# Kernel tuning notes

Measured on AMD Instinct MI355X. Metric: run time of the kernel, lower is better.

## Reference

```python
import jax, jax.numpy as jnp
import numpy as np

M = 0.25
GAMMA = 256.0
HARD_W = 2.0
O_P = 1.0 + M
O_N = -M
DELTA_P = 1.0 - M
DELTA_N = M
NEG_BIG = -1e30  # masked-out fill for logsumexp (finite to keep grads NaN-free)


def setup_inputs() -> dict:
    key = jax.random.key(0)
    k1, k2 = jax.random.split(key)
    inputs = jax.random.normal(k1, (4096, 512), dtype=jnp.float32)
    targets = jax.random.randint(k2, (4096,), 0, 64, dtype=jnp.int64)
    return {"inputs": inputs, "targets": targets}


def reference(inputs, targets):
    n = inputs.shape[0]
    x = inputs / jnp.linalg.norm(inputs, axis=1, keepdims=True)  # L2 normalize
    sim = x @ x.T                                                # [n, n]

    same = targets[:, None] == targets[None, :]
    eye = jnp.eye(n, dtype=bool)
    pos_mask = same & ~eye
    neg_mask = ~same
    npos = pos_mask.sum(axis=1)
    nneg = neg_mask.sum(axis=1)

    sim_d = jax.lax.stop_gradient(sim)  # alphas are detached in the original
    alpha_p = jax.nn.relu(O_P - sim_d)
    alpha_n = jax.nn.relu(sim_d - O_N)

    # hard mining: scale alpha at hardest positive (min sim) / hardest negative (max sim)
    idx = jnp.arange(n)
    hard_p = jnp.argmin(jnp.where(pos_mask, sim_d, jnp.inf), axis=1)
    hard_n = jnp.argmax(jnp.where(neg_mask, sim_d, -jnp.inf), axis=1)
    hit_p = (idx[None, :] == hard_p[:, None]) & (npos > 1)[:, None]
    hit_n = (idx[None, :] == hard_n[:, None]) & (nneg > 1)[:, None]
    alpha_p = alpha_p * jnp.where(hit_p, HARD_W, 1.0)
    alpha_n = alpha_n * jnp.where(hit_n, HARD_W, 1.0)

    pos_term = jnp.where(pos_mask, -GAMMA * alpha_p * (sim - DELTA_P), NEG_BIG)
    neg_term = jnp.where(neg_mask, GAMMA * alpha_n * (sim - DELTA_N), NEG_BIG)
    lse_p = jax.nn.logsumexp(pos_term, axis=1)
    lse_n = jax.nn.logsumexp(neg_term, axis=1)

    valid = (npos > 0) & (nneg > 0)
    per_row = jnp.where(valid, jax.nn.softplus(lse_p + lse_n), 0.0)
    n_valid = jnp.maximum(valid.sum(), 1)
    return per_row.sum() / n_valid.astype(per_row.dtype)
```

## Files before the change

### kernel.cpp

```cpp
#include <hip/hip_runtime.h>


#define GAMMA_ 256.0f
#define MASKT_  (-1.0e4f)
#define MINITP_ (-1.0e4f)
#define MASKP_  (-3.0e4f)

constexpr int N_ = 4096;
constexpr int D_ = 512;
constexpr int AST_ = 520;
constexpr int CCH_ = 16;

typedef __bf16 bf16x8 __attribute__((ext_vector_type(8)));
typedef float  f32x4  __attribute__((ext_vector_type(4)));
typedef const unsigned int __attribute__((address_space(1)))* gp_t;
typedef unsigned int       __attribute__((address_space(3)))* lp_t;

__device__ __forceinline__ float pos_q(float s) {
    float d = s - 1.0f;
    return fmaf(d * d, 256.0f, -16.0f);
}
__device__ __forceinline__ float neg_q(float s) {
    float q = fmaf(s * s, 256.0f, -16.0f);
    return (s >= -0.25f) ? q : 0.0f;
}
__device__ __forceinline__ void lse_merge(float m2, float S2, float& m, float& S) {
    float mm = fmaxf(m, m2);
    S = S * __expf(m - mm) + S2 * __expf(m2 - mm);
    m = mm;
}
__device__ __forceinline__ unsigned short f2bf(float f) {
    unsigned int u = __float_as_uint(f);
    unsigned int r = u + 0x7FFFu + ((u >> 16) & 1u);
    return (unsigned short)(r >> 16);
}

__global__ __launch_bounds__(256) void k_norm(const float* __restrict__ in,
                                              unsigned short* __restrict__ xb,
                                              float* __restrict__ acc) {
    const int row  = blockIdx.x * 4 + (threadIdx.x >> 6);
    const int lane = threadIdx.x & 63;
    const float4* src = (const float4*)(in + (size_t)row * D_) + lane * 2;
    float4 a = src[0], b = src[1];
    float ss = a.x*a.x + a.y*a.y + a.z*a.z + a.w*a.w
             + b.x*b.x + b.y*b.y + b.z*b.z + b.w*b.w;
    #pragma unroll
    for (int d = 32; d >= 1; d >>= 1) ss += __shfl_xor(ss, d);
    float rn = 1.0f / sqrtf(ss);
    float v[8] = {a.x, a.y, a.z, a.w, b.x, b.y, b.z, b.w};
    union { uint4 u; unsigned short us[8]; } pk;
    #pragma unroll
    for (int k = 0; k < 8; ++k) pk.us[k] = f2bf(v[k] * rn);
    *((uint4*)(xb + (size_t)row * D_) + lane) = pk.u;
    if (blockIdx.x == 0 && threadIdx.x < 2) acc[threadIdx.x] = 0.0f;
}

__global__ __launch_bounds__(256, 4) void k_mainD(const unsigned short* __restrict__ xb,
                                                  const int* __restrict__ tg,
                                                  float* __restrict__ part) {
    constexpr int NST = 16;
    __shared__ __align__(16) unsigned short Bs[2][16][AST_];

    const int tid  = threadIdx.x;
    const int wave = tid >> 6, lane = tid & 63;
    const int n16  = lane & 15, quad = lane >> 4;
    const int rg   = (int)blockIdx.x >> 4;
    const int cc   = (int)blockIdx.x & 15;
    const int rowBase = rg * 64 + wave * 16;
    const int colBase = cc * 256;

    bf16x8 af[16];
    {
        const bf16x8* ap = (const bf16x8*)(xb + (size_t)(rowBase + n16) * D_ + quad * 8);
        #pragma unroll
        for (int kk = 0; kk < 16; ++kk) af[kk] = ap[kk * 4];
    }
    int tr[4];
    #pragma unroll
    for (int r = 0; r < 4; ++r) tr[r] = tg[rowBase + quad * 4 + r];

    float m_p[4], S_p[4], m_n[4], S_n[4], mxn[4];
    #pragma unroll
    for (int r = 0; r < 4; ++r) {
        m_p[r] = MINITP_; S_p[r] = 0.f; m_n[r] = 0.f; S_n[r] = 0.f; mxn[r] = -2.0f;
    }

    const char* gstage = (const char*)xb + (size_t)colBase * 1024 + lane * 16;

    #pragma unroll
    for (int p = 0; p < 4; ++p) {
        int j = p * 4 + wave;
        __builtin_amdgcn_global_load_lds((gp_t)(const void*)(gstage + j * 1024),
                                         (lp_t)(void*)&Bs[0][j][0], 16, 0, 0);
    }
    int tc_cur = tg[colBase + n16];

    #pragma unroll 1
    for (int s = 0; s < NST; ++s) {
        const int b = s & 1;
        __syncthreads();

        if (s + 1 < NST) {
            const char* g2 = gstage + (size_t)(s + 1) * 16 * 1024;
            #pragma unroll
            for (int p = 0; p < 4; ++p) {
                int j = p * 4 + wave;
                __builtin_amdgcn_global_load_lds((gp_t)(const void*)(g2 + j * 1024),
                                                 (lp_t)(void*)&Bs[b ^ 1][j][0], 16, 0, 0);
            }
        }
        int tc_nxt = (s + 1 < NST) ? tg[colBase + (s + 1) * 16 + n16] : 0;

        f32x4 a0 = {0.f, 0.f, 0.f, 0.f}, a1 = {0.f, 0.f, 0.f, 0.f};
        #pragma unroll
        for (int kk = 0; kk < 8; ++kk) {
            bf16x8 bf0 = *(const bf16x8*)&Bs[b][n16][(2 * kk) * 32 + quad * 8];
            bf16x8 bf1 = *(const bf16x8*)&Bs[b][n16][(2 * kk + 1) * 32 + quad * 8];
            a0 = __builtin_amdgcn_mfma_f32_16x16x32_bf16(af[2 * kk],     bf0, a0, 0, 0, 0);
            a1 = __builtin_amdgcn_mfma_f32_16x16x32_bf16(af[2 * kk + 1], bf1, a1, 0, 0, 0);
        }

        const int jcol = colBase + s * 16 + n16;
        const int rd = jcol - rowBase - quad * 4;
        #pragma unroll
        for (int r = 0; r < 4; ++r) {
            float sim = a0[r] + a1[r];
            bool samec = (tr[r] == tc_cur);
            float d1 = sim - 1.0f;
            float tp = fmaf(d1 * d1, 256.0f, -16.0f);
            tp = (samec && rd != r) ? tp : MASKP_;
            float mm = fmaxf(m_p[r], tp);
            S_p[r] = S_p[r] * __expf(m_p[r] - mm) + __expf(tp - mm); m_p[r] = mm;
            float q = fmaf(sim * sim, 256.0f, -16.0f);
            q = (sim >= -0.25f) ? q : 0.0f;
            float tn = samec ? MASKT_ : q;
            mm = fmaxf(m_n[r], tn);
            S_n[r] = S_n[r] * __expf(m_n[r] - mm) + __expf(tn - mm); m_n[r] = mm;
            mxn[r] = fmaxf(mxn[r], samec ? -2.0f : sim);
        }
        tc_cur = tc_nxt;
    }

    #pragma unroll
    for (int r = 0; r < 4; ++r) {
        #pragma unroll
        for (int d = 1; d <= 8; d <<= 1) {
            lse_merge(__shfl_xor(m_p[r], d), __shfl_xor(S_p[r], d), m_p[r], S_p[r]);
            lse_merge(__shfl_xor(m_n[r], d), __shfl_xor(S_n[r], d), m_n[r], S_n[r]);
            mxn[r] = fmaxf(mxn[r], __shfl_xor(mxn[r], d));
        }
    }
    if (n16 == 0) {
        #pragma unroll
        for (int r = 0; r < 4; ++r) {
            ((float4*)part)[(size_t)(rowBase + quad * 4 + r) * CCH_ + cc] =
                make_float4(m_p[r], S_p[r], mxn[r], S_n[r]);
        }
    }
}

__global__ __launch_bounds__(256) void k_reduceD(const float* __restrict__ part,
                                                 const int* __restrict__ tg,
                                                 float* __restrict__ acc) {
    __shared__ int hist[64];
    const int tid = threadIdx.x;
    if (tid < 64) hist[tid] = 0;
    __syncthreads();
    for (int i = tid; i < N_; i += 256) atomicAdd(&hist[tg[i]], 1);
    __syncthreads();

    const int row = blockIdx.x * 256 + tid;
    const float4* P = (const float4*)part + (size_t)row * CCH_;
    float M_p = MINITP_, Sp = 0.f, M_n = 0.f, Sn = 0.f, mxn = -2.0f;
    #pragma unroll
    for (int c = 0; c < CCH_; ++c) {
        float4 a = P[c];
        lse_merge(a.x, a.y, M_p, Sp);
        float mn = (a.z > -1.5f) ? fmaxf(neg_q(a.z), 0.0f) : 0.0f;
        lse_merge(mn, a.w, M_n, Sn);
        mxn = fmaxf(mxn, a.z);
    }
    const int cnt = hist[tg[row]];
    float np2 = (float)(cnt - 1), nn2 = (float)(N_ - cnt);
    float loss = 0.f, vld = 0.f;
    if (np2 > 0.5f && nn2 > 0.5f) {
        if (np2 > 1.5f) {
            float t1 = M_p, t2 = 2.0f * t1;
            float mm = fmaxf(M_p, t2);
            Sp = Sp * __expf(M_p - mm) + __expf(t2 - mm) - __expf(t1 - mm);
            M_p = mm;
        }
        if (nn2 > 1.5f) {
            float t1 = neg_q(mxn), t2 = 2.0f * t1;
            float mm = fmaxf(M_n, t2);
            Sn = Sn * __expf(M_n - mm) + __expf(t2 - mm) - __expf(t1 - mm);
            M_n = mm;
        }
        float z = (M_p + __logf(Sp)) + (M_n + __logf(Sn));
        loss = fmaxf(z, 0.0f) + log1pf(__expf(-fabsf(z)));
        vld = 1.0f;
    }
    #pragma unroll
    for (int d = 32; d >= 1; d >>= 1) { loss += __shfl_xor(loss, d); vld += __shfl_xor(vld, d); }
    if ((tid & 63) == 0) { atomicAdd(&acc[0], loss); atomicAdd(&acc[1], vld); }
}

__global__ void k_final(const float* __restrict__ acc, float* __restrict__ out) {
    if (threadIdx.x == 0) out[0] = acc[0] / fmaxf(acc[1], 1.0f);
}

__global__ void k_sentinel(float* __restrict__ out) {
    if (threadIdx.x == 0) out[0] = -12345.0f;
}

__global__ __launch_bounds__(1024, 4) void k_main3(const unsigned short* __restrict__ xb,
                                                   const int* __restrict__ tg,
                                                   float* __restrict__ acc_g) {
    __shared__ __align__(16) unsigned short As[16 * AST_];
    __shared__ float sm[16][16][8];
    const int tid  = threadIdx.x;
    const int wave = tid >> 6, lane = tid & 63;
    const int n16  = lane & 15, quad = lane >> 4;
    const int rowBase = blockIdx.x * 16;
    {
        int row = tid >> 6, c = tid & 63;
        *(uint4*)&As[row * AST_ + c * 8] =
            *(const uint4*)(xb + (size_t)(rowBase + row) * D_ + c * 8);
    }
    int ir[4], tr[4];
    #pragma unroll
    for (int r = 0; r < 4; ++r) { ir[r] = rowBase + quad * 4 + r; tr[r] = tg[ir[r]]; }
    float m_p[4], S_p[4], m_n[4], S_n[4], mnp[4], mxn[4], sc[4];
    #pragma unroll
    for (int r = 0; r < 4; ++r) {
        m_p[r] = 0.f; S_p[r] = 0.f; m_n[r] = 0.f; S_n[r] = 0.f;
        mnp[r] = 2.0f; mxn[r] = -2.0f; sc[r] = 0.f;
    }
    __syncthreads();
    const unsigned short* Af = &As[n16 * AST_ + quad * 8];
    #pragma unroll 1
    for (int t = wave; t < N_ / 16; t += 16) {
        const int jcol = t * 16 + n16;
        const int tc = tg[jcol];
        const bf16x8* bp = (const bf16x8*)(xb + (size_t)jcol * D_ + quad * 8);
        bf16x8 bf[16];
        #pragma unroll
        for (int kk = 0; kk < 16; ++kk) bf[kk] = bp[kk * 4];
        f32x4 a0 = {0.f, 0.f, 0.f, 0.f}, a1 = {0.f, 0.f, 0.f, 0.f};
        #pragma unroll
        for (int kk = 0; kk < 8; ++kk) {
            bf16x8 af0 = *(const bf16x8*)(Af + (2 * kk) * 32);
            bf16x8 af1 = *(const bf16x8*)(Af + (2 * kk + 1) * 32);
            a0 = __builtin_amdgcn_mfma_f32_16x16x32_bf16(af0, bf[2 * kk],     a0, 0, 0, 0);
            a1 = __builtin_amdgcn_mfma_f32_16x16x32_bf16(af1, bf[2 * kk + 1], a1, 0, 0, 0);
        }
        #pragma unroll
        for (int r = 0; r < 4; ++r) {
            float s = a0[r] + a1[r];
            bool samec = (tr[r] == tc);
            bool posm  = samec && (jcol != ir[r]);
            float tp = posm  ? pos_q(s) : MASKT_;
            float tn = samec ? MASKT_ : neg_q(s);
            float mm = fmaxf(m_p[r], tp);
            S_p[r] = S_p[r] * __expf(m_p[r] - mm) + __expf(tp - mm); m_p[r] = mm;
            mm = fmaxf(m_n[r], tn);
            S_n[r] = S_n[r] * __expf(m_n[r] - mm) + __expf(tn - mm); m_n[r] = mm;
            sc[r] += samec ? 1.0f : 0.0f;
            mnp[r] = fminf(mnp[r], posm ? s : 2.0f);
            mxn[r] = fmaxf(mxn[r], samec ? -2.0f : s);
        }
    }
    #pragma unroll
    for (int r = 0; r < 4; ++r) {
        #pragma unroll
        for (int d = 1; d <= 8; d <<= 1) {
            lse_merge(__shfl_xor(m_p[r], d), __shfl_xor(S_p[r], d), m_p[r], S_p[r]);
            lse_merge(__shfl_xor(m_n[r], d), __shfl_xor(S_n[r], d), m_n[r], S_n[r]);
            mnp[r] = fminf(mnp[r], __shfl_xor(mnp[r], d));
            mxn[r] = fmaxf(mxn[r], __shfl_xor(mxn[r], d));
            sc[r] += __shfl_xor(sc[r], d);
        }
    }
    if (n16 == 0) {
        #pragma unroll
        for (int r = 0; r < 4; ++r) {
            float* q = sm[wave][quad * 4 + r];
            q[0] = m_p[r]; q[1] = S_p[r]; q[2] = m_n[r]; q[3] = S_n[r];
            q[4] = mnp[r]; q[5] = mxn[r]; q[6] = sc[r];
        }
    }
    __syncthreads();
    if (tid < 64) {
        const int L = tid & 15;
        float m_p2 = 0.f, S_p2 = 0.f, m_n2 = 0.f, S_n2 = 0.f;
        float mnp2 = 2.0f, mxn2 = -2.0f, sct = 0.f;
        #pragma unroll
        for (int w = 0; w < 16; ++w) {
            const float* q = sm[w][L];
            lse_merge(q[0], q[1], m_p2, S_p2);
            lse_merge(q[2], q[3], m_n2, S_n2);
            mnp2 = fminf(mnp2, q[4]); mxn2 = fmaxf(mxn2, q[5]);
            sct += q[6];
        }
        float loss = 0.f, vld = 0.f;
        float np2 = sct - 1.0f, nn2 = (float)N_ - sct;
        if (tid < 16 && np2 > 0.5f && nn2 > 0.5f) {
            if (np2 > 1.5f) {
                float t1 = pos_q(mnp2), t2 = 2.0f * t1;
                float mm = fmaxf(m_p2, t2);
                S_p2 = S_p2 * __expf(m_p2 - mm) + __expf(t2 - mm) - __expf(t1 - mm);
                m_p2 = mm;
            }
            if (nn2 > 1.5f) {
                float t1 = neg_q(mxn2), t2 = 2.0f * t1;
                float mm = fmaxf(m_n2, t2);
                S_n2 = S_n2 * __expf(m_n2 - mm) + __expf(t2 - mm) - __expf(t1 - mm);
                m_n2 = mm;
            }
            float z = (m_p2 + __logf(S_p2)) + (m_n2 + __logf(S_n2));
            loss = fmaxf(z, 0.0f) + log1pf(__expf(-fabsf(z)));
            vld = 1.0f;
        }
        #pragma unroll
        for (int d = 32; d >= 1; d >>= 1) {
            loss += __shfl_xor(loss, d); vld += __shfl_xor(vld, d);
        }
        if (tid == 0) { atomicAdd(&acc_g[0], loss); atomicAdd(&acc_g[1], vld); }
    }
}

extern "C" void kernel_launch(void* const* d_in, const int* in_sizes, int n_in,
                              void* d_out, int out_size, void* d_ws, size_t ws_size,
                              hipStream_t stream) {
    const float* in = (const float*)d_in[0];
    const int*   tg = (const int*)d_in[1];
    constexpr size_t MB = 1024 * 1024;
    unsigned short* xb = (unsigned short*)d_ws;

    if (ws_size >= 5 * MB + 64) {
        float* part = (float*)((char*)d_ws + 4 * MB);
        float* acc  = (float*)((char*)d_ws + 5 * MB);
        hipLaunchKernelGGL(k_norm,    dim3(N_ / 4),    dim3(256), 0, stream, in, xb, acc);
        hipLaunchKernelGGL(k_mainD,   dim3(64 * CCH_), dim3(256), 0, stream, xb, tg, part);
        hipLaunchKernelGGL(k_reduceD, dim3(N_ / 256),  dim3(256), 0, stream, part, tg, acc);
        hipLaunchKernelGGL(k_final,   dim3(1),         dim3(64),  0, stream, acc, (float*)d_out);
    } else if (ws_size >= 4 * MB + 64) {
        float* acc = (float*)((char*)d_ws + 4 * MB);
        hipLaunchKernelGGL(k_norm,  dim3(N_ / 4),  dim3(256),  0, stream, in, xb, acc);
        hipLaunchKernelGGL(k_main3, dim3(N_ / 16), dim3(1024), 0, stream, xb, tg, acc);
        hipLaunchKernelGGL(k_final, dim3(1),       dim3(64),   0, stream, acc, (float*)d_out);
    } else {
        hipLaunchKernelGGL(k_sentinel, dim3(1), dim3(64), 0, stream, (float*)d_out);
    }
}
```

Before: 107.9 us.

## Compute two 16-row tiles per wave and merge pos/neg online-softmax into one exp

Each wave now covers 32 rows instead of 16, reusing every B fragment loaded from LDS for two MFMA row tiles. This halves the grid and the LDS/global traffic for B per output, at the cost of doubling A-fragment registers and lowering occupancy (launch bounds 4 to 2). The epilogue also drops the two separate online-logsumexp updates and uses one branch-selected update per element, since each element is either a positive or a negative, so only one exp is computed. The data-dependent branch may diverge within a wave.

```diff
diff --git a/kernel.cpp b/kernel.cpp
--- a/kernel.cpp
+++ b/kernel.cpp
@@ -55,7 +55,7 @@
     if (blockIdx.x == 0 && threadIdx.x < 2) acc[threadIdx.x] = 0.0f;
 }
 
-__global__ __launch_bounds__(256, 4) void k_mainD(const unsigned short* __restrict__ xb,
+__global__ __launch_bounds__(256, 2) void k_mainE(const unsigned short* __restrict__ xb,
                                                   const int* __restrict__ tg,
                                                   float* __restrict__ part) {
     constexpr int NST = 16;
@@ -66,23 +66,27 @@
     const int n16  = lane & 15, quad = lane >> 4;
     const int rg   = (int)blockIdx.x >> 4;
     const int cc   = (int)blockIdx.x & 15;
-    const int rowBase = rg * 64 + wave * 16;
+    const int rowBase = rg * 128 + wave * 32;
     const int colBase = cc * 256;
 
-    bf16x8 af[16];
+    bf16x8 af0[16], af1[16];
     {
-        const bf16x8* ap = (const bf16x8*)(xb + (size_t)(rowBase + n16) * D_ + quad * 8);
-        #pragma unroll
-        for (int kk = 0; kk < 16; ++kk) af[kk] = ap[kk * 4];
-    }
-    int tr[4];
-    #pragma unroll
-    for (int r = 0; r < 4; ++r) tr[r] = tg[rowBase + quad * 4 + r];
-
-    float m_p[4], S_p[4], m_n[4], S_n[4], mxn[4];
-    #pragma unroll
-    for (int r = 0; r < 4; ++r) {
-        m_p[r] = MINITP_; S_p[r] = 0.f; m_n[r] = 0.f; S_n[r] = 0.f; mxn[r] = -2.0f;
+        const bf16x8* a0p = (const bf16x8*)(xb + (size_t)(rowBase + n16) * D_ + quad * 8);
+        const bf16x8* a1p = (const bf16x8*)(xb + (size_t)(rowBase + 16 + n16) * D_ + quad * 8);
+        #pragma unroll
+        for (int kk = 0; kk < 16; ++kk) { af0[kk] = a0p[kk * 4]; af1[kk] = a1p[kk * 4]; }
+    }
+    int tr[8];
+    #pragma unroll
+    for (int t = 0; t < 2; ++t)
+        #pragma unroll
+        for (int r = 0; r < 4; ++r)
+            tr[t * 4 + r] = tg[rowBase + t * 16 + quad * 4 + r];
+
+    float m_p[8], S_p[8], m_n[8], S_n[8], mxn[8];
+    #pragma unroll
+    for (int i = 0; i < 8; ++i) {
+        m_p[i] = MINITP_; S_p[i] = 0.f; m_n[i] = 0.f; S_n[i] = 0.f; mxn[i] = -2.0f;
     }
 
     const char* gstage = (const char*)xb + (size_t)colBase * 1024 + lane * 16;
@@ -111,51 +115,67 @@
         }
         int tc_nxt = (s + 1 < NST) ? tg[colBase + (s + 1) * 16 + n16] : 0;
 
-        f32x4 a0 = {0.f, 0.f, 0.f, 0.f}, a1 = {0.f, 0.f, 0.f, 0.f};
+        f32x4 A00 = {0.f,0.f,0.f,0.f}, A01 = {0.f,0.f,0.f,0.f};
+        f32x4 A10 = {0.f,0.f,0.f,0.f}, A11 = {0.f,0.f,0.f,0.f};
         #pragma unroll
         for (int kk = 0; kk < 8; ++kk) {
             bf16x8 bf0 = *(const bf16x8*)&Bs[b][n16][(2 * kk) * 32 + quad * 8];
             bf16x8 bf1 = *(const bf16x8*)&Bs[b][n16][(2 * kk + 1) * 32 + quad * 8];
-            a0 = __builtin_amdgcn_mfma_f32_16x16x32_bf16(af[2 * kk],     bf0, a0, 0, 0, 0);
-            a1 = __builtin_amdgcn_mfma_f32_16x16x32_bf16(af[2 * kk + 1], bf1, a1, 0, 0, 0);
+            A00 = __builtin_amdgcn_mfma_f32_16x16x32_bf16(af0[2 * kk],     bf0, A00, 0, 0, 0);
+            A10 = __builtin_amdgcn_mfma_f32_16x16x32_bf16(af1[2 * kk],     bf0, A10, 0, 0, 0);
+            A01 = __builtin_amdgcn_mfma_f32_16x16x32_bf16(af0[2 * kk + 1], bf1, A01, 0, 0, 0);
+            A11 = __builtin_amdgcn_mfma_f32_16x16x32_bf16(af1[2 * kk + 1], bf1, A11, 0, 0, 0);
         }
 
         const int jcol = colBase + s * 16 + n16;
         const int rd = jcol - rowBase - quad * 4;
         #pragma unroll
-        for (int r = 0; r < 4; ++r) {
-            float sim = a0[r] + a1[r];
-            bool samec = (tr[r] == tc_cur);
-            float d1 = sim - 1.0f;
-            float tp = fmaf(d1 * d1, 256.0f, -16.0f);
-            tp = (samec && rd != r) ? tp : MASKP_;
-            float mm = fmaxf(m_p[r], tp);
-            S_p[r] = S_p[r] * __expf(m_p[r] - mm) + __expf(tp - mm); m_p[r] = mm;
-            float q = fmaf(sim * sim, 256.0f, -16.0f);
-            q = (sim >= -0.25f) ? q : 0.0f;
-            float tn = samec ? MASKT_ : q;
-            mm = fmaxf(m_n[r], tn);
-            S_n[r] = S_n[r] * __expf(m_n[r] - mm) + __expf(tn - mm); m_n[r] = mm;
-            mxn[r] = fmaxf(mxn[r], samec ? -2.0f : sim);
+        for (int t = 0; t < 2; ++t) {
+            #pragma unroll
+            for (int r = 0; r < 4; ++r) {
+                const int i = t * 4 + r;
+                float sim = (t == 0) ? (A00[r] + A01[r]) : (A10[r] + A11[r]);
+                bool samec = (tr[i] == tc_cur);
+                bool diag  = (rd == t * 16 + r);
+                float d1 = sim - 1.0f;
+                float tp = fmaf(d1 * d1, 256.0f, -16.0f);
+                float q  = fmaf(sim * sim, 256.0f, -16.0f);
+                float tn = (sim >= -0.25f) ? q : 0.0f;
+                float tv = samec ? (diag ? MASKP_ : tp) : tn;
+                float ms = samec ? m_p[i] : m_n[i];
+                if (tv > ms) {
+                    float scl = __expf(ms - tv);
+                    if (samec) { S_p[i] = fmaf(S_p[i], scl, 1.0f); m_p[i] = tv; }
+                    else       { S_n[i] = fmaf(S_n[i], scl, 1.0f); m_n[i] = tv; }
+                } else {
+                    float e = __expf(tv - ms);
+                    S_p[i] += samec ? e : 0.0f;
+                    S_n[i] += samec ? 0.0f : e;
+                }
+                mxn[i] = fmaxf(mxn[i], samec ? -2.0f : sim);
+            }
         }
         tc_cur = tc_nxt;
     }
 
     #pragma unroll
-    for (int r = 0; r < 4; ++r) {
+    for (int i = 0; i < 8; ++i) {
         #pragma unroll
         for (int d = 1; d <= 8; d <<= 1) {
-            lse_merge(__shfl_xor(m_p[r], d), __shfl_xor(S_p[r], d), m_p[r], S_p[r]);
-            lse_merge(__shfl_xor(m_n[r], d), __shfl_xor(S_n[r], d), m_n[r], S_n[r]);
-            mxn[r] = fmaxf(mxn[r], __shfl_xor(mxn[r], d));
+            lse_merge(__shfl_xor(m_p[i], d), __shfl_xor(S_p[i], d), m_p[i], S_p[i]);
+            lse_merge(__shfl_xor(m_n[i], d), __shfl_xor(S_n[i], d), m_n[i], S_n[i]);
+            mxn[i] = fmaxf(mxn[i], __shfl_xor(mxn[i], d));
         }
     }
     if (n16 == 0) {
         #pragma unroll
-        for (int r = 0; r < 4; ++r) {
-            ((float4*)part)[(size_t)(rowBase + quad * 4 + r) * CCH_ + cc] =
-                make_float4(m_p[r], S_p[r], mxn[r], S_n[r]);
-        }
+        for (int t = 0; t < 2; ++t)
+            #pragma unroll
+            for (int r = 0; r < 4; ++r) {
+                const int i = t * 4 + r;
+                ((float4*)part)[(size_t)(rowBase + t * 16 + quad * 4 + r) * CCH_ + cc] =
+                    make_float4(m_p[i], S_p[i], mxn[i], S_n[i]);
+            }
     }
 }
 
@@ -341,7 +361,7 @@
         float* part = (float*)((char*)d_ws + 4 * MB);
         float* acc  = (float*)((char*)d_ws + 5 * MB);
         hipLaunchKernelGGL(k_norm,    dim3(N_ / 4),    dim3(256), 0, stream, in, xb, acc);
-        hipLaunchKernelGGL(k_mainD,   dim3(64 * CCH_), dim3(256), 0, stream, xb, tg, part);
+        hipLaunchKernelGGL(k_mainE,   dim3(32 * CCH_), dim3(256), 0, stream, xb, tg, part);
         hipLaunchKernelGGL(k_reduceD, dim3(N_ / 256),  dim3(256), 0, stream, part, tg, acc);
         hipLaunchKernelGGL(k_final,   dim3(1),         dim3(64),  0, stream, acc, (float*)d_out);
     } else if (ws_size >= 4 * MB + 64) {
```

Result: slower. 112.2 us (+4.0%).
